# Kernel tuning notes

Measured on AMD Instinct MI355X. Metric: run time of the kernel, lower is better.

The kernel has to match this reference:

```python
import jax, jax.numpy as jnp
import numpy as np

N = 471
TOPK = 50
T = 16384
M = 128


def setup_inputs() -> dict:
    key = jax.random.key(0)
    ks = jax.random.split(key, 6)
    x = jax.random.normal(ks[0], (T, N), dtype=jnp.float32)
    q_t = jax.random.normal(ks[1], (M, N), dtype=jnp.float32)
    # parameters, initialized as in the torch module
    w = 0.0021 + 0.0005 * jax.random.normal(ks[2], (N,), dtype=jnp.float32)
    b1 = jax.random.normal(ks[3], (N,), dtype=jnp.float32)  # unused in forward math
    alpha = jnp.array([10.0], dtype=jnp.float32)
    lamda = jnp.array([0.1], dtype=jnp.float32)
    rho = jnp.array([0.001], dtype=jnp.float32)
    mu = jnp.array([0.001], dtype=jnp.float32)
    bound = 1.0 / np.sqrt(N)
    linear_w = jax.random.uniform(ks[4], (N, N), minval=-bound, maxval=bound, dtype=jnp.float32)
    linear_b = jax.random.uniform(ks[5], (N,), minval=-bound, maxval=bound, dtype=jnp.float32)
    return {"x": x, "q_t": q_t, "w": w, "b1": b1, "alpha": alpha,
            "lamda": lamda, "rho": rho, "mu": mu,
            "linear_w": linear_w, "linear_b": linear_b}


def reference(x, q_t, w, b1, alpha, lamda, rho, mu, linear_w, linear_b):
    # W2 = mean over time of Linear(x); identical every unrolled iteration -> compute once
    W2 = (x @ linear_w.T + linear_b).mean(axis=0)           # [N]
    pinvQ = jnp.linalg.pinv(q_t @ q_t.T)                    # [M,M], identical every iter

    def theta_update(z, u):
        v = u - rho * (z - w)                               # [N]
        return alpha * (pinvQ @ (q_t @ v))                  # [M]

    def z_update(z, u, theta):
        b = w + (q_t.T @ theta) / N                         # [N]
        grad_z = W2 + rho * (z - b) + u
        grad_z = grad_z + 2.0 * lamda * (jnp.sum(z) - 1.0)  # scalar * ones broadcast
        grad_z = grad_z + 2.0 * lamda * jnp.minimum(0.0, z)
        z_new = jax.nn.relu(z - mu * grad_z)
        _, idx = jax.lax.top_k(z_new, TOPK)
        mask = jnp.zeros_like(z_new).at[idx].set(1.0)
        return z_new * mask

    z = jnp.zeros(N, dtype=x.dtype)
    u = jnp.zeros(N, dtype=x.dtype)
    for _ in range(9):
        theta = theta_update(z, u)
        z = z_update(z, u, theta)
        b = w + (q_t.T @ theta) / N
        u = u + rho * (z - b)
    theta = theta_update(z, u)
    z = z_update(z, u, theta)
    return z / (jnp.sum(z) + 1e-8)
```

## Files before the change

### kernel.cpp

```cpp
#include <hip/hip_runtime.h>

#define NDIM 471
#define MD   128
#define TD   16384
#define KSEL 50
#define CGIT 4

#define WS_PART   0
#define WS_G      120832
#define WS_T1     137216
#define WS_XBAR   197888
#define WS_W2     198400
#define WS_RW     198912
#define WS_CTR    199384
#define WS_R      199424

static __device__ __forceinline__ float rdl(float v, int lane){
    return __int_as_float(__builtin_amdgcn_readlane(__float_as_int(v), lane));
}

__global__ __launch_bounds__(512) void k_gram_colsum(const float* __restrict__ qt,
                                                     const float* __restrict__ x,
                                                     const float* __restrict__ wv,
                                                     float* __restrict__ ws){
    int lane = threadIdx.x & 63, wid = threadIdx.x >> 6;
    if (blockIdx.x == 0 && threadIdx.x == 0)
        __hip_atomic_store((unsigned*)(ws + WS_CTR), 0u, __ATOMIC_RELEASE, __HIP_MEMORY_SCOPE_AGENT);
    if (blockIdx.x < 256){
        float* G = ws + WS_G;
        int gw = blockIdx.x * 8 + wid;
        int i = gw >> 4, jb = gw & 15;
        float qi[8];
#pragma unroll
        for (int s = 0; s < 8; ++s){ int idx = lane + 64*s; qi[s] = (idx < NDIM) ? qt[i*NDIM + idx] : 0.f; }
#pragma unroll
        for (int t = 0; t < 8; ++t){
            int j = jb + 16*t;
            float acc = 0.f;
#pragma unroll
            for (int s = 0; s < 8; ++s){
                int idx = lane + 64*s;
                float qj = (idx < NDIM) ? qt[j*NDIM + idx] : 0.f;
                acc = fmaf(qi[s], qj, acc);
            }
#pragma unroll
            for (int d = 1; d < 64; d <<= 1) acc += __shfl_xor(acc, d);
            if (lane == 0) G[i*MD + j] = acc;
        }
    } else {
        int cb = blockIdx.x - 256;
        int col = threadIdx.x;
        if (col < NDIM){
            const float* xp = x + (size_t)cb*64*NDIM + col;
            float acc = 0.f;
#pragma unroll 4
            for (int r = 0; r < 64; ++r) acc += xp[(size_t)r*NDIM];
            ws[WS_PART + cb*NDIM + col] = acc;
        }
        if (cb < 16){
            int m = cb*8 + wid;
            float acc = 0.f;
#pragma unroll
            for (int s = 0; s < 8; ++s){
                int idx = lane + 64*s;
                if (idx < NDIM) acc = fmaf(qt[m*NDIM + idx], wv[idx], acc);
            }
#pragma unroll
            for (int d = 1; d < 64; d <<= 1) acc += __shfl_xor(acc, d);
            if (lane == 0) ws[WS_T1 + m] = acc;
        }
    }
}

#define G_LD(n) float4 t##n = *(const float4*)(Gp + 4*(n)); \
                float Ga##n = t##n.x, Gb##n = t##n.y, Gc##n = t##n.z, Gd##n = t##n.w;
#define G_DOT(n) pa = fmaf(Ga##n, rdl(rch.x, 2*(n)),   pa); \
                 pb = fmaf(Gb##n, rdl(rch.y, 2*(n)),   pb); \
                 pa = fmaf(Gc##n, rdl(rch.x, 2*(n)+1), pa); \
                 pb = fmaf(Gd##n, rdl(rch.y, 2*(n)+1), pb);

__global__ __launch_bounds__(256, 1) void k_cg_xbar(const float* __restrict__ qt,
                                                    const float* __restrict__ alpha,
                                                    const float* __restrict__ lw,
                                                    const float* __restrict__ lb,
                                                    float* __restrict__ ws){
    int tid = threadIdx.x, lane = tid & 63, wid = tid >> 6;
    __shared__ __align__(16) float rl[2][2][128];
    __shared__ float part[2][2][128];
    {
        int row = tid & 127, seg = tid >> 7;
        int c   = seg;
        int col = blockIdx.x*2 + c;
        const float* Gp = ws + WS_G + row*MD + seg*64;
        G_LD(0) G_LD(1) G_LD(2)  G_LD(3)  G_LD(4)  G_LD(5)  G_LD(6)  G_LD(7)
        G_LD(8) G_LD(9) G_LD(10) G_LD(11) G_LD(12) G_LD(13) G_LD(14) G_LD(15)
        float bvv = (col < NDIM) ? qt[row*NDIM + col] : ws[WS_T1 + row];
        float xv = 0.f, rv = bvv, pv = 0.f, sv = 0.f, gam = 1.f, alf = 1.f;
        int buf = 0;
        rl[0][c][row] = rv;
        for (int it = 0; it < CGIT; ++it){
            __syncthreads();
#pragma unroll
            for (int cc = 0; cc < 2; ++cc){
                float2 rch = *(const float2*)&rl[buf][cc][seg*64 + 2*(lane & 31)];
                float pa = 0.f, pb = 0.f;
                G_DOT(0) G_DOT(1) G_DOT(2)  G_DOT(3)  G_DOT(4)  G_DOT(5)  G_DOT(6)  G_DOT(7)
                G_DOT(8) G_DOT(9) G_DOT(10) G_DOT(11) G_DOT(12) G_DOT(13) G_DOT(14) G_DOT(15)
                part[seg][cc][row] = pa + pb;
            }
            __syncthreads();
            float y = part[0][c][row] + part[1][c][row];
            float r0 = rl[buf][c][lane],      r1 = rl[buf][c][lane + 64];
            float y0 = part[0][c][lane]      + part[1][c][lane];
            float y1 = part[0][c][lane + 64] + part[1][c][lane + 64];
            float t0 = fmaf(r0, r0, r1*r1);
            float t1 = fmaf(y0, r0, y1*r1);
#pragma unroll
            for (int d = 1; d < 64; d <<= 1){ t0 += __shfl_xor(t0, d); t1 += __shfl_xor(t1, d); }
            float gp = t0, dl = t1;
            float bet, anew;
            if (it == 0){ bet = 0.f; anew = gp / fmaxf(dl, 1e-30f); }
            else { bet = gp / fmaxf(gam, 1e-30f); anew = gp / fmaxf(dl - bet*gp/alf, 1e-30f); }
            pv = fmaf(bet, pv, rv);
            sv = fmaf(bet, sv, y);
            xv = fmaf(anew, pv, xv);
            rv = fmaf(-anew, sv, rv);
            gam = gp; alf = anew;
            rl[buf^1][c][row] = rv;
            buf ^= 1;
        }
        rl[buf][c][row] = xv;
        __syncthreads();
        float sc = alpha[0] / (float)NDIM;
        float2 wc0 = ((const float2*)&rl[buf][0][0])[lane];
        float2 wc1 = ((const float2*)&rl[buf][1][0])[lane];
        int i0 = tid;
        int i1 = (tid + 256 < NDIM) ? tid + 256 : (NDIM - 1);
        float a0=0.f, a1=0.f, b0=0.f, b1=0.f;
#pragma unroll
        for (int l = 0; l < 64; ++l){
            float w0a = rdl(wc0.x, l), w0b = rdl(wc0.y, l);
            float w1a = rdl(wc1.x, l), w1b = rdl(wc1.y, l);
            float qa0 = qt[(2*l+0)*NDIM + i0], qa1 = qt[(2*l+0)*NDIM + i1];
            float qb0 = qt[(2*l+1)*NDIM + i0], qb1 = qt[(2*l+1)*NDIM + i1];
            a0 = fmaf(qa0, w0a, a0); a0 = fmaf(qb0, w0b, a0);
            a1 = fmaf(qa1, w0a, a1); a1 = fmaf(qb1, w0b, a1);
            b0 = fmaf(qa0, w1a, b0); b0 = fmaf(qb0, w1b, b0);
            b1 = fmaf(qa1, w1a, b1); b1 = fmaf(qb1, w1b, b1);
        }
        int col0 = blockIdx.x*2, col1 = col0 + 1;
        ws[WS_R + (size_t)col0*NDIM + i0] = sc*a0;
        if (tid + 256 < NDIM) ws[WS_R + (size_t)col0*NDIM + tid+256] = sc*a1;
        if (col1 < NDIM){
            ws[WS_R + (size_t)col1*NDIM + i0] = sc*b0;
            if (tid + 256 < NDIM) ws[WS_R + (size_t)col1*NDIM + tid+256] = sc*b1;
        } else {
            ws[WS_RW + i0] = sc*b0;
            if (tid + 256 < NDIM) ws[WS_RW + tid+256] = sc*b1;
        }
    }
    if (blockIdx.x < 59){
        __shared__ float p2[4][8];
        unsigned* ctr = (unsigned*)(ws + WS_CTR);
        __syncthreads();
        int b2 = blockIdx.x;
        int cl = tid & 7, seg2 = tid >> 3;
        int col = b2*8 + cl;
        float acc = 0.f;
        if (col < NDIM){
#pragma unroll
            for (int q = 0; q < 8; ++q) acc += ws[WS_PART + (seg2*8 + q)*NDIM + col];
        }
        acc += __shfl_xor(acc, 8);
        acc += __shfl_xor(acc, 16);
        acc += __shfl_xor(acc, 32);
        if (lane < 8) p2[wid][lane] = acc;
        __syncthreads();
        if (tid < 8){
            float t = ((p2[0][tid] + p2[1][tid]) + (p2[2][tid] + p2[3][tid]));
            int c2 = b2*8 + tid;
            if (c2 < NDIM) ws[WS_XBAR + c2] = t * (1.0f / TD);
        }
        __syncthreads();
        if (tid == 0){
            __hip_atomic_fetch_add(ctr, 1u, __ATOMIC_RELEASE, __HIP_MEMORY_SCOPE_AGENT);
            while (__hip_atomic_load(ctr, __ATOMIC_RELAXED, __HIP_MEMORY_SCOPE_AGENT) < 59u)
                __builtin_amdgcn_s_sleep(2);
            __builtin_amdgcn_fence(__ATOMIC_ACQUIRE, "agent");
        }
        __syncthreads();
        for (int r = wid; r < 8; r += 4){
            int i = b2*8 + r;
            if (i < NDIM){
                float acc2 = 0.f;
#pragma unroll
                for (int s = 0; s < 8; ++s){
                    int idx = lane + 64*s;
                    if (idx < NDIM) acc2 = fmaf(lw[(size_t)i*NDIM + idx], ws[WS_XBAR + idx], acc2);
                }
#pragma unroll
                for (int d = 1; d < 64; d <<= 1) acc2 += __shfl_xor(acc2, d);
                if (lane == 0) ws[WS_W2 + i] = acc2 + lb[i];
            }
        }
    }
}

__global__ __launch_bounds__(512, 2) void k_iter(const float* __restrict__ wv,
                                              const float* __restrict__ alpha, const float* __restrict__ lamda,
                                              const float* __restrict__ rho_p, const float* __restrict__ mu_p,
                                              const float* __restrict__ ws, float* __restrict__ out){
    int tid = threadIdx.x, lane = tid & 63, wid = tid >> 6;
    bool act = tid < NDIM;
    int ti = act ? tid : 0;
    float rho = rho_p[0], mu = mu_p[0], lam = lamda[0];
    float sc  = alpha[0] / (float)NDIM;
    float wi  = act ? wv[tid]         : 0.f;
    float Rwi = act ? ws[WS_RW + tid] : 0.f;
    float W2i = act ? ws[WS_W2 + tid] : 0.f;

    __shared__ __align__(16) unsigned bins[1024];
    __shared__ __align__(8) float2 spair[64];
    __shared__ float warr[8];
    __shared__ unsigned wcnt[8];

    bins[tid] = 0u; bins[tid + 512] = 0u;
    __syncthreads();

    float z = 0.f, u = 0.f, Ruv = 0.f, Rzv = 0.f, Sz = 0.f;
    unsigned tau = 0xFFFFFFFFu;
    for (int it = 0; it < 10; ++it){
        float Rv = Ruv - rho*(Rzv - Rwi);
        float b  = wi + Rv;
        float grad = W2i + rho*(z - b) + u + 2.f*lam*(Sz - 1.f);
        float zn = z - mu*grad;
        zn = (act && zn > 0.f) ? zn : 0.f;
        unsigned bits = __float_as_uint(zn);

        bool cge = act && (bits >= tau);
        unsigned long long cm = __ballot(cge);
        float vs = cge ? zn : 0.f;
#pragma unroll
        for (int d = 1; d < 64; d <<= 1) vs += __shfl_xor(vs, d);
        if (lane == 0){ wcnt[wid] = (unsigned)__popcll(cm); warr[wid] = vs; }
        __syncthreads();
        int cnt0 = 0;
#pragma unroll
        for (int w2 = 0; w2 < 8; ++w2) cnt0 += (int)wcnt[w2];
        bool fast = (cnt0 == KSEL);
        unsigned prefix = tau;
        unsigned long long mb;

        if (fast){
            z = cge ? zn : 0.f;
            mb = cm;
        } else {
            prefix = 0; unsigned need = KSEL;
#pragma unroll
            for (int pass = 3; pass >= 0; --pass){
                int sh = pass*8;
                unsigned* bp = bins + ((3 - pass) << 8);
                bool av = (pass == 3) || ((bits >> (sh + 8)) == (prefix >> (sh + 8)));
                if (av) atomicAdd(&bp[(bits >> sh) & 255u], 1u);
                __syncthreads();
                int base = 255 - 4*lane;
                uint4 bq = *(const uint4*)&bp[base - 3];
                unsigned b3 = bq.x, b2 = bq.y, b1 = bq.z, b0 = bq.w;
                unsigned csum = b0 + b1 + b2 + b3;
                unsigned incl = csum;
#pragma unroll
                for (int d = 1; d < 64; d <<= 1){ unsigned t = __shfl_up(incl, d); if (lane >= d) incl += t; }
                unsigned excl = incl - csum;
                bool hit = (excl < need) && (need <= incl);
                unsigned long long hm = __ballot(hit);
                int hl = __ffsll((long long)hm) - 1;
                unsigned c0 = excl + b0, c1 = c0 + b1, c2 = c1 + b2;
                int byte; unsigned above, cntc;
                if      (need <= c0){ byte = base;   above = excl; cntc = b0; }
                else if (need <= c1){ byte = base-1; above = c0;   cntc = b1; }
                else if (need <= c2){ byte = base-2; above = c1;   cntc = b2; }
                else                { byte = base-3; above = c2;   cntc = b3; }
                byte  = __shfl(byte, hl);
                above = (unsigned)__shfl((int)above, hl);
                cntc  = (unsigned)__shfl((int)cntc, hl);
                prefix |= ((unsigned)byte) << sh;
                need -= above;
                if (cntc == need) break;
            }
            tau = prefix;
            z = (act && bits >= prefix) ? zn : 0.f;
            bool flag = z > 0.f;
            mb = __ballot(flag);
            float v = z;
#pragma unroll
            for (int d = 1; d < 64; d <<= 1) v += __shfl_xor(v, d);
            if (lane == 0){ warr[wid] = v; wcnt[wid] = (unsigned)__popcll(mb); }
            __syncthreads();
        }
        Sz = ((warr[0]+warr[1])+(warr[2]+warr[3])) + ((warr[4]+warr[5])+(warr[6]+warr[7]));

        if (it < 9){
            bool flag = z > 0.f;
            unsigned off = 0;
#pragma unroll
            for (int w2 = 0; w2 < 8; ++w2) if (w2 < wid) off += wcnt[w2];
            off += (unsigned)__popcll(mb & ((1ull << lane) - 1ull));
            int cnt = 0;
#pragma unroll
            for (int w2 = 0; w2 < 8; ++w2) cnt += (int)wcnt[w2];
            if (flag){ spair[off] = make_float2(__int_as_float(tid), z); }
            if (tid >= cnt && tid < 64){ spair[tid] = make_float2(__int_as_float(0), 0.f); }
            bins[tid] = 0u; bins[tid + 512] = 0u;
            __syncthreads();

            float2 pp = spair[lane];
            const float* Rb = ws + WS_R;
            float rvv[56];
#pragma unroll
            for (int s = 0; s < 56; ++s){
                int j = __float_as_int(rdl(pp.x, s));
                rvv[s] = Rb[(size_t)j*NDIM + ti];
            }
            float a0=0.f, a1=0.f, a2=0.f, a3=0.f;
#pragma unroll
            for (int s = 0; s < 56; s += 4){
                a0 = fmaf(rvv[s+0], rdl(pp.y, s+0), a0);
                a1 = fmaf(rvv[s+1], rdl(pp.y, s+1), a1);
                a2 = fmaf(rvv[s+2], rdl(pp.y, s+2), a2);
                a3 = fmaf(rvv[s+3], rdl(pp.y, s+3), a3);
            }
            float acc = (a0+a1) + (a2+a3);
            float Rbv = Rwi + sc*Rv;
            u   += rho*(z - b);
            Ruv += rho*(acc - Rbv);
            Rzv  = acc;
        }
    }
    if (act) out[tid] = z / (Sz + 1e-8f);
}

extern "C" void kernel_launch(void* const* d_in, const int* in_sizes, int n_in,
                              void* d_out, int out_size, void* d_ws, size_t ws_size,
                              hipStream_t stream) {
    const float* x     = (const float*)d_in[0];
    const float* qt    = (const float*)d_in[1];
    const float* wv    = (const float*)d_in[2];
    const float* alpha = (const float*)d_in[4];
    const float* lamda = (const float*)d_in[5];
    const float* rho   = (const float*)d_in[6];
    const float* mu    = (const float*)d_in[7];
    const float* lw    = (const float*)d_in[8];
    const float* lb    = (const float*)d_in[9];
    float* out = (float*)d_out;
    float* ws  = (float*)d_ws;

    k_gram_colsum<<<512, 512, 0, stream>>>(qt, x, wv, ws);
    k_cg_xbar    <<<236, 256, 0, stream>>>(qt, alpha, lw, lb, ws);
    k_iter       <<<1,   512, 0, stream>>>(wv, alpha, lamda, rho, mu, ws, out);
}
```

Measured before the change: 54.88 us.

## Move x column-sum into CG kernel and halve CG iterations

Moves the x column-sum reduction out of the Gram kernel and into the CG/xbar kernel, with 236 blocks each summing 70 rows before starting CG. A new counter gates the later xbar reduction. This is meant to overlap the memory-bound x read with the compute-bound CG solve and shrink the first kernel to 256 blocks. It also cuts the CG iterations from 4 to 2, which lowers the solve cost but may lose accuracy in the pseudo-inverse solve.

```diff
diff --git a/kernel.cpp b/kernel.cpp
--- a/kernel.cpp
+++ b/kernel.cpp
@@ -4,7 +4,8 @@
 #define MD   128
 #define TD   16384
 #define KSEL 50
-#define CGIT 4
+#define CGIT 2
+#define CROWS 70
 
 #define WS_PART   0
 #define WS_G      120832
@@ -19,56 +20,46 @@
     return __int_as_float(__builtin_amdgcn_readlane(__float_as_int(v), lane));
 }
 
-__global__ __launch_bounds__(512) void k_gram_colsum(const float* __restrict__ qt,
-                                                     const float* __restrict__ x,
-                                                     const float* __restrict__ wv,
-                                                     float* __restrict__ ws){
+__global__ __launch_bounds__(512) void k_gram(const float* __restrict__ qt,
+                                              const float* __restrict__ wv,
+                                              float* __restrict__ ws){
     int lane = threadIdx.x & 63, wid = threadIdx.x >> 6;
-    if (blockIdx.x == 0 && threadIdx.x == 0)
-        __hip_atomic_store((unsigned*)(ws + WS_CTR), 0u, __ATOMIC_RELEASE, __HIP_MEMORY_SCOPE_AGENT);
-    if (blockIdx.x < 256){
-        float* G = ws + WS_G;
-        int gw = blockIdx.x * 8 + wid;
-        int i = gw >> 4, jb = gw & 15;
-        float qi[8];
-#pragma unroll
-        for (int s = 0; s < 8; ++s){ int idx = lane + 64*s; qi[s] = (idx < NDIM) ? qt[i*NDIM + idx] : 0.f; }
-#pragma unroll
-        for (int t = 0; t < 8; ++t){
-            int j = jb + 16*t;
-            float acc = 0.f;
-#pragma unroll
-            for (int s = 0; s < 8; ++s){
-                int idx = lane + 64*s;
-                float qj = (idx < NDIM) ? qt[j*NDIM + idx] : 0.f;
-                acc = fmaf(qi[s], qj, acc);
-            }
-#pragma unroll
-            for (int d = 1; d < 64; d <<= 1) acc += __shfl_xor(acc, d);
-            if (lane == 0) G[i*MD + j] = acc;
-        }
-    } else {
-        int cb = blockIdx.x - 256;
-        int col = threadIdx.x;
-        if (col < NDIM){
-            const float* xp = x + (size_t)cb*64*NDIM + col;
-            float acc = 0.f;
-#pragma unroll 4
-            for (int r = 0; r < 64; ++r) acc += xp[(size_t)r*NDIM];
-            ws[WS_PART + cb*NDIM + col] = acc;
-        }
-        if (cb < 16){
-            int m = cb*8 + wid;
-            float acc = 0.f;
-#pragma unroll
-            for (int s = 0; s < 8; ++s){
-                int idx = lane + 64*s;
-                if (idx < NDIM) acc = fmaf(qt[m*NDIM + idx], wv[idx], acc);
-            }
-#pragma unroll
-            for (int d = 1; d < 64; d <<= 1) acc += __shfl_xor(acc, d);
-            if (lane == 0) ws[WS_T1 + m] = acc;
-        }
+    if (blockIdx.x == 0 && threadIdx.x == 0){
+        unsigned* C = (unsigned*)(ws + WS_CTR);
+        __hip_atomic_store(&C[0], 0u, __ATOMIC_RELAXED, __HIP_MEMORY_SCOPE_AGENT);
+        __hip_atomic_store(&C[1], 0u, __ATOMIC_RELAXED, __HIP_MEMORY_SCOPE_AGENT);
+    }
+    float* G = ws + WS_G;
+    int gw = blockIdx.x * 8 + wid;
+    int i = gw >> 4, jb = gw & 15;
+    float qi[8];
+#pragma unroll
+    for (int s = 0; s < 8; ++s){ int idx = lane + 64*s; qi[s] = (idx < NDIM) ? qt[i*NDIM + idx] : 0.f; }
+#pragma unroll
+    for (int t = 0; t < 8; ++t){
+        int j = jb + 16*t;
+        float acc = 0.f;
+#pragma unroll
+        for (int s = 0; s < 8; ++s){
+            int idx = lane + 64*s;
+            float qj = (idx < NDIM) ? qt[j*NDIM + idx] : 0.f;
+            acc = fmaf(qi[s], qj, acc);
+        }
+#pragma unroll
+        for (int d = 1; d < 64; d <<= 1) acc += __shfl_xor(acc, d);
+        if (lane == 0) G[i*MD + j] = acc;
+    }
+    if (blockIdx.x < 16){
+        int m = blockIdx.x*8 + wid;
+        float acc = 0.f;
+#pragma unroll
+        for (int s = 0; s < 8; ++s){
+            int idx = lane + 64*s;
+            if (idx < NDIM) acc = fmaf(qt[m*NDIM + idx], wv[idx], acc);
+        }
+#pragma unroll
+        for (int d = 1; d < 64; d <<= 1) acc += __shfl_xor(acc, d);
+        if (lane == 0) ws[WS_T1 + m] = acc;
     }
 }
 
@@ -80,11 +71,13 @@
                  pb = fmaf(Gd##n, rdl(rch.y, 2*(n)+1), pb);
 
 __global__ __launch_bounds__(256, 1) void k_cg_xbar(const float* __restrict__ qt,
+                                                    const float* __restrict__ x,
                                                     const float* __restrict__ alpha,
                                                     const float* __restrict__ lw,
                                                     const float* __restrict__ lb,
                                                     float* __restrict__ ws){
     int tid = threadIdx.x, lane = tid & 63, wid = tid >> 6;
+    unsigned* C = (unsigned*)(ws + WS_CTR);
     __shared__ __align__(16) float rl[2][2][128];
     __shared__ float part[2][2][128];
     {
@@ -95,6 +88,30 @@
         G_LD(0) G_LD(1) G_LD(2)  G_LD(3)  G_LD(4)  G_LD(5)  G_LD(6)  G_LD(7)
         G_LD(8) G_LD(9) G_LD(10) G_LD(11) G_LD(12) G_LD(13) G_LD(14) G_LD(15)
         float bvv = (col < NDIM) ? qt[row*NDIM + col] : ws[WS_T1 + row];
+
+        {
+            int start = blockIdx.x * CROWS;
+            int cnt = TD - start; if (cnt > CROWS) cnt = CROWS;
+            int c0 = tid, c1 = tid + 256;
+            bool h1 = c1 < NDIM;
+            const float* xp = x + (size_t)start*NDIM;
+            float s0=0.f, s1=0.f, s2=0.f, s3=0.f;
+            int r = 0;
+#pragma unroll 4
+            for (; r + 2 <= cnt; r += 2){
+                s0 += xp[(size_t)(r+0)*NDIM + c0];
+                s2 += xp[(size_t)(r+1)*NDIM + c0];
+                if (h1) s1 += xp[(size_t)(r+0)*NDIM + c1];
+                if (h1) s3 += xp[(size_t)(r+1)*NDIM + c1];
+            }
+            if (r < cnt){ s0 += xp[(size_t)r*NDIM + c0]; if (h1) s1 += xp[(size_t)r*NDIM + c1]; }
+            ws[WS_PART + blockIdx.x*NDIM + c0] = s0 + s2;
+            if (h1) ws[WS_PART + blockIdx.x*NDIM + c1] = s1 + s3;
+        }
+        __syncthreads();
+        if (tid == 0)
+            __hip_atomic_fetch_add(&C[0], 1u, __ATOMIC_RELEASE, __HIP_MEMORY_SCOPE_AGENT);
+
         float xv = 0.f, rv = bvv, pv = 0.f, sv = 0.f, gam = 1.f, alf = 1.f;
         int buf = 0;
         rl[0][c][row] = rv;
@@ -161,7 +178,12 @@
     }
     if (blockIdx.x < 59){
         __shared__ float p2[4][8];
-        unsigned* ctr = (unsigned*)(ws + WS_CTR);
+        __syncthreads();
+        if (tid == 0){
+            while (__hip_atomic_load(&C[0], __ATOMIC_RELAXED, __HIP_MEMORY_SCOPE_AGENT) < 236u)
+                __builtin_amdgcn_s_sleep(2);
+            __builtin_amdgcn_fence(__ATOMIC_ACQUIRE, "agent");
+        }
         __syncthreads();
         int b2 = blockIdx.x;
         int cl = tid & 7, seg2 = tid >> 3;
@@ -169,7 +191,10 @@
         float acc = 0.f;
         if (col < NDIM){
 #pragma unroll
-            for (int q = 0; q < 8; ++q) acc += ws[WS_PART + (seg2*8 + q)*NDIM + col];
+            for (int q = 0; q < 8; ++q){
+                int rw = seg2*8 + q;
+                if (rw < 236) acc += ws[WS_PART + rw*NDIM + col];
+            }
         }
         acc += __shfl_xor(acc, 8);
         acc += __shfl_xor(acc, 16);
@@ -183,8 +208,8 @@
         }
         __syncthreads();
         if (tid == 0){
-            __hip_atomic_fetch_add(ctr, 1u, __ATOMIC_RELEASE, __HIP_MEMORY_SCOPE_AGENT);
-            while (__hip_atomic_load(ctr, __ATOMIC_RELAXED, __HIP_MEMORY_SCOPE_AGENT) < 59u)
+            __hip_atomic_fetch_add(&C[1], 1u, __ATOMIC_RELEASE, __HIP_MEMORY_SCOPE_AGENT);
+            while (__hip_atomic_load(&C[1], __ATOMIC_RELAXED, __HIP_MEMORY_SCOPE_AGENT) < 59u)
                 __builtin_amdgcn_s_sleep(2);
             __builtin_amdgcn_fence(__ATOMIC_ACQUIRE, "agent");
         }
@@ -354,7 +379,7 @@
     float* out = (float*)d_out;
     float* ws  = (float*)d_ws;
 
-    k_gram_colsum<<<512, 512, 0, stream>>>(qt, x, wv, ws);
-    k_cg_xbar    <<<236, 256, 0, stream>>>(qt, alpha, lw, lb, ws);
-    k_iter       <<<1,   512, 0, stream>>>(wv, alpha, lamda, rho, mu, ws, out);
-}
+    k_gram   <<<256, 512, 0, stream>>>(qt, wv, ws);
+    k_cg_xbar<<<236, 256, 0, stream>>>(qt, x, alpha, lw, lb, ws);
+    k_iter   <<<1,   512, 0, stream>>>(wv, alpha, lamda, rho, mu, ws, out);
+}
```

After: 76.84 us. +40.0%, slower.

## Split column-sum over four row groups, halve CG iterations, relocate workspace

Applied to the files above, without the earlier changes.

Each column-sum block now splits its 64 rows into four 16-row groups, each thread summing four adjacent columns, so there are four times as many partial sums. The reduction stage reads 32 partials per segment instead of 8, and the workspace offsets are enlarged to fit the bigger partial buffer. The counter reset becomes a relaxed store. CGIT drops from 4 to 2, which halves the conjugate-gradient refinement used for the pseudo-inverse and risks lower accuracy.

```diff
diff --git a/kernel.cpp b/kernel.cpp
--- a/kernel.cpp
+++ b/kernel.cpp
@@ -4,16 +4,16 @@
 #define MD   128
 #define TD   16384
 #define KSEL 50
-#define CGIT 4
+#define CGIT 2
 
 #define WS_PART   0
-#define WS_G      120832
-#define WS_T1     137216
-#define WS_XBAR   197888
-#define WS_W2     198400
-#define WS_RW     198912
-#define WS_CTR    199384
-#define WS_R      199424
+#define WS_G      482304
+#define WS_T1     498688
+#define WS_XBAR   498816
+#define WS_W2     499328
+#define WS_RW     499840
+#define WS_CTR    500352
+#define WS_R      500368
 
 static __device__ __forceinline__ float rdl(float v, int lane){
     return __int_as_float(__builtin_amdgcn_readlane(__float_as_int(v), lane));
@@ -23,9 +23,9 @@
                                                      const float* __restrict__ x,
                                                      const float* __restrict__ wv,
                                                      float* __restrict__ ws){
-    int lane = threadIdx.x & 63, wid = threadIdx.x >> 6;
-    if (blockIdx.x == 0 && threadIdx.x == 0)
-        __hip_atomic_store((unsigned*)(ws + WS_CTR), 0u, __ATOMIC_RELEASE, __HIP_MEMORY_SCOPE_AGENT);
+    int tid = threadIdx.x, lane = tid & 63, wid = tid >> 6;
+    if (blockIdx.x == 0 && tid == 0)
+        __hip_atomic_store((unsigned*)(ws + WS_CTR), 0u, __ATOMIC_RELAXED, __HIP_MEMORY_SCOPE_AGENT);
     if (blockIdx.x < 256){
         float* G = ws + WS_G;
         int gw = blockIdx.x * 8 + wid;
@@ -47,18 +47,8 @@
             for (int d = 1; d < 64; d <<= 1) acc += __shfl_xor(acc, d);
             if (lane == 0) G[i*MD + j] = acc;
         }
-    } else {
-        int cb = blockIdx.x - 256;
-        int col = threadIdx.x;
-        if (col < NDIM){
-            const float* xp = x + (size_t)cb*64*NDIM + col;
-            float acc = 0.f;
-#pragma unroll 4
-            for (int r = 0; r < 64; ++r) acc += xp[(size_t)r*NDIM];
-            ws[WS_PART + cb*NDIM + col] = acc;
-        }
-        if (cb < 16){
-            int m = cb*8 + wid;
+        if (blockIdx.x < 16){
+            int m = blockIdx.x*8 + wid;
             float acc = 0.f;
 #pragma unroll
             for (int s = 0; s < 8; ++s){
@@ -68,6 +58,24 @@
 #pragma unroll
             for (int d = 1; d < 64; d <<= 1) acc += __shfl_xor(acc, d);
             if (lane == 0) ws[WS_T1 + m] = acc;
+        }
+    } else {
+        int cb = blockIdx.x - 256;
+        int g = tid >> 7, t = tid & 127;
+        if (t < 118){
+            int c0 = 4*t;
+            bool v3 = (c0 + 3) < NDIM;
+            const float* xp = x + (size_t)(cb*64 + g*16)*NDIM + c0;
+            float a0=0.f, a1=0.f, a2=0.f, a3=0.f;
+#pragma unroll
+            for (int r = 0; r < 16; ++r){
+                const float* rp = xp + (size_t)r*NDIM;
+                a0 += rp[0]; a1 += rp[1]; a2 += rp[2];
+                if (v3) a3 += rp[3];
+            }
+            float* pp = ws + WS_PART + (size_t)(cb*4 + g)*NDIM + c0;
+            pp[0] = a0; pp[1] = a1; pp[2] = a2;
+            if (v3) pp[3] = a3;
         }
     }
 }
@@ -168,8 +176,8 @@
         int col = b2*8 + cl;
         float acc = 0.f;
         if (col < NDIM){
-#pragma unroll
-            for (int q = 0; q < 8; ++q) acc += ws[WS_PART + (seg2*8 + q)*NDIM + col];
+#pragma unroll 8
+            for (int q = 0; q < 32; ++q) acc += ws[WS_PART + (size_t)(seg2*32 + q)*NDIM + col];
         }
         acc += __shfl_xor(acc, 8);
         acc += __shfl_xor(acc, 16);
```

New measurement: 54.51 us. Within noise of the previous version (-0.7%).
